# Performance work log

Hardware: AMD Instinct MI355X
Metric: run time of the kernel (lower is better)

The kernel has to match this reference:

```python
import jax, jax.numpy as jnp
import numpy as np

EMBED_DIM = 768
N_HEADS = 12
HEAD_DIM = EMBED_DIM // N_HEADS
B, S = 8, 1024


def setup_inputs() -> dict:
    key = jax.random.key(0)
    ks = jax.random.split(key, 7)
    sc = 1.0 / np.sqrt(HEAD_DIM)
    return {
        "sequences": jax.random.normal(ks[0], (B, S, EMBED_DIM), dtype=jnp.float32),
        # per-head Linear weights stored [H, in, out] (torch Linear is x @ W.T + b;
        # with random init the layout convention is equivalent math)
        "Wq": jax.random.normal(ks[1], (N_HEADS, HEAD_DIM, HEAD_DIM), dtype=jnp.float32) * sc,
        "bq": jax.random.normal(ks[2], (N_HEADS, HEAD_DIM), dtype=jnp.float32) * 0.01,
        "Wk": jax.random.normal(ks[3], (N_HEADS, HEAD_DIM, HEAD_DIM), dtype=jnp.float32) * sc,
        "bk": jax.random.normal(ks[4], (N_HEADS, HEAD_DIM), dtype=jnp.float32) * 0.01,
        "Wv": jax.random.normal(ks[5], (N_HEADS, HEAD_DIM, HEAD_DIM), dtype=jnp.float32) * sc,
        "bv": jax.random.normal(ks[6], (N_HEADS, HEAD_DIM), dtype=jnp.float32) * 0.01,
    }


def reference(sequences, Wq, bq, Wk, bk, Wv, bv):
    b, s, d = sequences.shape
    h, hd = Wq.shape[0], Wq.shape[1]
    x = sequences.reshape(b, s, h, hd)              # split embed dim into heads
    q = jnp.einsum("bshd,hde->bshe", x, Wq) + bq    # per-head linear (block-diag GEMM)
    k = jnp.einsum("bshd,hde->bshe", x, Wk) + bk
    v = jnp.einsum("bshd,hde->bshe", x, Wv) + bv
    # NOTE: original module applies NO 1/sqrt(head_dim) scaling
    logits = jnp.einsum("bshe,bthe->bhst", q, k)    # [B,H,S,S]
    attn = jax.nn.softmax(logits, axis=-1)
    out = jnp.einsum("bhst,bthe->bshe", attn, v)    # [B,S,H,hd]
    return out.reshape(b, s, d)
```

## Files before the change

kernel.cpp:

```cpp
#include <hip/hip_runtime.h>
#include <stdint.h>

#define EMBED 768
#define NH 12
#define HD 64
#define Bsz 8
#define Ssz 1024
#define LOG2E 1.44269504088896f

typedef __attribute__((ext_vector_type(4))) float f32x4;
typedef __attribute__((ext_vector_type(8))) _Float16 f16x8;
typedef __attribute__((ext_vector_type(4))) _Float16 f16x4;
typedef __attribute__((ext_vector_type(2))) _Float16 f16x2;

__device__ __forceinline__ int SW(int row, int col) {
    return row * 64 + (col ^ ((row & 7) << 3));
}

__launch_bounds__(256)
__global__ void qkv_proj(const float* __restrict__ x,
                         const float* __restrict__ Wq, const float* __restrict__ bq,
                         const float* __restrict__ Wk, const float* __restrict__ bk,
                         const float* __restrict__ Wv, const float* __restrict__ bv,
                         _Float16* __restrict__ Qb, _Float16* __restrict__ Kb,
                         _Float16* __restrict__ Vt)
{
    __shared__ _Float16 XT[128 * 72];
    __shared__ _Float16 Wt[3 * 64 * 72];
    __shared__ float Bs[192];

    const int bt = blockIdx.x;
    const int st = bt & 7;
    const int h  = (bt >> 3) % NH;
    const int b  = bt / (8 * NH);
    const int sbase = st * 128;
    const int tid = threadIdx.x;
    const int lane = tid & 63, w = tid >> 6;
    const int l15 = lane & 15, quad = lane >> 4;

    for (int i = 0; i < 8; ++i) {
        int idx = tid + 256 * i;
        int row = idx >> 4;
        int c4  = (idx & 15) * 4;
        const float4 g = *(const float4*)&x[(size_t)(b * Ssz + sbase + row) * EMBED + h * HD + c4];
        f16x4 v; v[0] = (_Float16)g.x; v[1] = (_Float16)g.y; v[2] = (_Float16)g.z; v[3] = (_Float16)g.w;
        *(f16x4*)&XT[row * 72 + c4] = v;
    }
    {
        const float* Ws0[3] = {Wq, Wk, Wv};
        const float* bs0[3] = {bq, bk, bv};
#pragma unroll
        for (int m = 0; m < 3; ++m) {
            const float* W = Ws0[m] + (size_t)h * HD * HD;
            for (int i = 0; i < 4; ++i) {
                int idx = tid + 256 * i;
                int d = idx >> 4, e4 = (idx & 15) * 4;
                float4 g = *(const float4*)&W[d * 64 + e4];
                Wt[m * 4608 + (e4 + 0) * 72 + d] = (_Float16)g.x;
                Wt[m * 4608 + (e4 + 1) * 72 + d] = (_Float16)g.y;
                Wt[m * 4608 + (e4 + 2) * 72 + d] = (_Float16)g.z;
                Wt[m * 4608 + (e4 + 3) * 72 + d] = (_Float16)g.w;
            }
        }
        if (tid < 192) Bs[tid] = bs0[tid >> 6][h * HD + (tid & 63)];
    }
    __syncthreads();

    f16x8 bx[2][2];
    const int nbg0 = w * 2;
#pragma unroll
    for (int nb = 0; nb < 2; ++nb)
#pragma unroll
        for (int kh = 0; kh < 2; ++kh)
            bx[nb][kh] = *(const f16x8*)&XT[((nbg0 + nb) * 16 + l15) * 72 + kh * 32 + quad * 8];
    __syncthreads();

    const size_t qkbase = (size_t)(b * NH + h) * Ssz + sbase;
    const f32x4 zero = {0.f, 0.f, 0.f, 0.f};

#pragma unroll
    for (int m = 0; m < 3; ++m) {
        f32x4 acc[2][4];
#pragma unroll
        for (int nb = 0; nb < 2; ++nb)
#pragma unroll
            for (int eb = 0; eb < 4; ++eb) acc[nb][eb] = zero;
#pragma unroll
        for (int eb = 0; eb < 4; ++eb)
#pragma unroll
            for (int kh = 0; kh < 2; ++kh) {
                f16x8 aw = *(const f16x8*)&Wt[m * 4608 + (eb * 16 + l15) * 72 + kh * 32 + quad * 8];
#pragma unroll
                for (int nb = 0; nb < 2; ++nb)
                    acc[nb][eb] = __builtin_amdgcn_mfma_f32_16x16x32_f16(aw, bx[nb][kh], acc[nb][eb], 0, 0, 0);
            }

        if (m < 2) {
            const float sc = (m == 0) ? LOG2E : 1.0f;
#pragma unroll
            for (int nb = 0; nb < 2; ++nb)
#pragma unroll
                for (int eb = 0; eb < 4; ++eb) {
                    f32x4 bb = *(const f32x4*)&Bs[m * 64 + eb * 16 + quad * 4];
                    f16x4 v;
#pragma unroll
                    for (int r = 0; r < 4; ++r) v[r] = (_Float16)((acc[nb][eb][r] + bb[r]) * sc);
                    *(f16x4*)&XT[((nbg0 + nb) * 16 + l15) * 72 + eb * 16 + quad * 4] = v;
                }
            __syncthreads();
            _Float16* outp = (m == 0) ? Qb : Kb;
            for (int i = 0; i < 4; ++i) {
                int idx = tid + 256 * i;
                int s = idx >> 3, e8 = (idx & 7) * 8;
                *(f16x8*)&outp[(qkbase + s) * HD + e8] = *(const f16x8*)&XT[s * 72 + e8];
            }
            __syncthreads();
        } else {
            _Float16* Vs = XT;
#pragma unroll
            for (int nb = 0; nb < 2; ++nb)
#pragma unroll
                for (int eb = 0; eb < 4; ++eb) {
                    f32x4 bb = *(const f32x4*)&Bs[128 + eb * 16 + quad * 4];
#pragma unroll
                    for (int r = 0; r < 4; ++r)
                        Vs[(eb * 16 + quad * 4 + r) * 136 + (nbg0 + nb) * 16 + l15] =
                            (_Float16)(acc[nb][eb][r] + bb[r]);
                }
            __syncthreads();
            for (int i = 0; i < 4; ++i) {
                int idx = tid + 256 * i;
                int e = idx >> 4, s8 = (idx & 15) * 8;
                *(f16x8*)&Vt[((size_t)(b * NH + h) * 64 + e) * Ssz + sbase + s8] =
                    *(const f16x8*)&Vs[e * 136 + s8];
            }
        }
    }
}

__launch_bounds__(512)
__global__ void attn(const _Float16* __restrict__ Qb, const _Float16* __restrict__ Kb,
                     const _Float16* __restrict__ Vt, float* __restrict__ out)
{
    __shared__ _Float16 KV[2 * 8192];
    __shared__ _Float16 Pl[8 * 16 * 64];

    const int bt = blockIdx.x;
    const int hh = bt % 96;
    const int qt = bt / 96;
    const int h  = hh % NH;
    const int b  = hh / NH;

    const int tid = threadIdx.x;
    const int lane = tid & 63, w = tid >> 6;
    const int l15 = lane & 15, quad = lane >> 4;

    const size_t bh = (size_t)(b * NH + h);
    const _Float16* Qg = Qb + bh * Ssz * HD;
    const _Float16* Kg = Kb + bh * Ssz * HD;
    const _Float16* Vg = Vt + bh * (size_t)HD * Ssz;

    const int qrow0 = qt * 128 + w * 16;
    f16x8 aq[2];
#pragma unroll
    for (int kh = 0; kh < 2; ++kh)
        aq[kh] = *(const f16x8*)&Qg[(qrow0 + l15) * HD + kh * 32 + quad * 8];

    const f32x4 zero = {0.f, 0.f, 0.f, 0.f};
    f32x4 o[4];
#pragma unroll
    for (int eb = 0; eb < 4; ++eb) o[eb] = zero;
    float m_run = -INFINITY, l_run = 0.f;

    const int srow = tid >> 3;
    const int scol = (tid & 7) * 8;
    const int swst = SW(srow, scol);

    f16x8 kr = *(const f16x8*)&Kg[srow * HD + scol];
    f16x8 vr = *(const f16x8*)&Vg[(size_t)srow * Ssz + scol];
    *(f16x8*)&KV[swst] = kr;
    *(f16x8*)&KV[4096 + swst] = vr;
    __syncthreads();

    _Float16* Pw = &Pl[w * 1024];
    const int swq = (l15 & 7) << 3;

    for (int kt = 0; kt < 16; ++kt) {
        const int cur = kt & 1;
        if (kt < 15) {
            kr = *(const f16x8*)&Kg[((kt + 1) * 64 + srow) * HD + scol];
            vr = *(const f16x8*)&Vg[(size_t)srow * Ssz + (kt + 1) * 64 + scol];
        }
        const _Float16* Ksb = &KV[cur * 8192];
        const _Float16* Vsb = &KV[cur * 8192 + 4096];

        f32x4 st[4];
#pragma unroll
        for (int tb = 0; tb < 4; ++tb) {
            f32x4 acc = zero;
#pragma unroll
            for (int kh = 0; kh < 2; ++kh) {
                f16x8 ak = *(const f16x8*)&Ksb[SW(tb * 16 + l15, kh * 32 + quad * 8)];
                acc = __builtin_amdgcn_mfma_f32_16x16x32_f16(ak, aq[kh], acc, 0, 0, 0);
            }
            st[tb] = acc;
        }

        float mt = st[0][0];
#pragma unroll
        for (int tb = 0; tb < 4; ++tb)
#pragma unroll
            for (int r = 0; r < 4; ++r) mt = fmaxf(mt, st[tb][r]);
        mt = fmaxf(mt, __shfl_xor(mt, 16, 64));
        mt = fmaxf(mt, __shfl_xor(mt, 32, 64));
        float mn = fmaxf(m_run, mt);
        float al = __builtin_amdgcn_exp2f(m_run - mn);
        float rs = 0.f;
        f16x4 pv[4];
#pragma unroll
        for (int tb = 0; tb < 4; ++tb) {
            float p0 = __builtin_amdgcn_exp2f(st[tb][0] - mn);
            float p1 = __builtin_amdgcn_exp2f(st[tb][1] - mn);
            float p2 = __builtin_amdgcn_exp2f(st[tb][2] - mn);
            float p3 = __builtin_amdgcn_exp2f(st[tb][3] - mn);
            rs += (p0 + p1) + (p2 + p3);
            f16x2 lo = __builtin_bit_cast(f16x2, __builtin_amdgcn_cvt_pkrtz(p0, p1));
            f16x2 hi = __builtin_bit_cast(f16x2, __builtin_amdgcn_cvt_pkrtz(p2, p3));
            pv[tb][0] = lo[0]; pv[tb][1] = lo[1]; pv[tb][2] = hi[0]; pv[tb][3] = hi[1];
        }
        rs += __shfl_xor(rs, 16, 64);
        rs += __shfl_xor(rs, 32, 64);
        l_run = l_run * al + rs;
        m_run = mn;
#pragma unroll
        for (int eb = 0; eb < 4; ++eb) o[eb] *= al;

#pragma unroll
        for (int tb = 0; tb < 4; ++tb)
            *(f16x4*)&Pw[l15 * 64 + ((tb * 16 + quad * 4) ^ swq)] = pv[tb];
        __asm__ __volatile__("s_waitcnt lgkmcnt(0)" ::: "memory");
        f16x8 bp[2];
#pragma unroll
        for (int kh = 0; kh < 2; ++kh)
            bp[kh] = *(const f16x8*)&Pw[l15 * 64 + ((kh * 32 + quad * 8) ^ swq)];

#pragma unroll
        for (int kh = 0; kh < 2; ++kh)
#pragma unroll
            for (int eb = 0; eb < 4; ++eb) {
                f16x8 av = *(const f16x8*)&Vsb[SW(eb * 16 + l15, kh * 32 + quad * 8)];
                o[eb] = __builtin_amdgcn_mfma_f32_16x16x32_f16(av, bp[kh], o[eb], 0, 0, 0);
            }

        if (kt < 15) {
            const int nxt = cur ^ 1;
            *(f16x8*)&KV[nxt * 8192 + swst] = kr;
            *(f16x8*)&KV[nxt * 8192 + 4096 + swst] = vr;
        }
        __syncthreads();
    }

    const float inv = 1.f / l_run;
    const int q = qrow0 + l15;
    float* op = &out[(size_t)(b * Ssz + q) * EMBED + h * HD + quad * 4];
#pragma unroll
    for (int eb = 0; eb < 4; ++eb) {
        f32x4 r = o[eb] * inv;
        *(f32x4*)&op[eb * 16] = r;
    }
}

extern "C" void kernel_launch(void* const* d_in, const int* in_sizes, int n_in,
                              void* d_out, int out_size, void* d_ws, size_t ws_size,
                              hipStream_t stream) {
    const float* x  = (const float*)d_in[0];
    const float* Wq = (const float*)d_in[1];
    const float* bq = (const float*)d_in[2];
    const float* Wk = (const float*)d_in[3];
    const float* bk = (const float*)d_in[4];
    const float* Wv = (const float*)d_in[5];
    const float* bv = (const float*)d_in[6];

    _Float16* Qb = (_Float16*)d_ws;
    _Float16* Kb = Qb + (size_t)Bsz * NH * Ssz * HD;
    _Float16* Vt = Kb + (size_t)Bsz * NH * Ssz * HD;

    qkv_proj<<<dim3(Bsz * NH * 8), dim3(256), 0, stream>>>(x, Wq, bq, Wk, bk, Wv, bv, Qb, Kb, Vt);
    attn<<<dim3(Bsz * NH * 8), dim3(512), 0, stream>>>(Qb, Kb, Vt, (float*)d_out);
}
```

Before: 136.7 us.

## Compute softmax row sums via extra MFMA ones-row and move KV stores earlier

Replaces the explicit per-row softmax sum (adds plus cross-lane shuffles) with a fifth MFMA against a ones row appended to the V tile in shared memory, so the denominator accumulates in o[4]. It also moves the next-tile K/V shared-memory stores before the P-read wait, so they can overlap with the PV MFMAs. The cost is an extra MFMA per k-half per tile, larger LDS buffers, and the sum is now taken over fp16-rounded probabilities rather than fp32 ones.

```diff
diff --git a/kernel.cpp b/kernel.cpp
--- a/kernel.cpp
+++ b/kernel.cpp
@@ -138,11 +138,12 @@
     }
 }
 
+#define KVBUF 9216
 __launch_bounds__(512)
 __global__ void attn(const _Float16* __restrict__ Qb, const _Float16* __restrict__ Kb,
                      const _Float16* __restrict__ Vt, float* __restrict__ out)
 {
-    __shared__ _Float16 KV[2 * 8192];
+    __shared__ _Float16 KV[2 * KVBUF];
     __shared__ _Float16 Pl[8 * 16 * 64];
 
     const int bt = blockIdx.x;
@@ -167,14 +168,24 @@
         aq[kh] = *(const f16x8*)&Qg[(qrow0 + l15) * HD + kh * 32 + quad * 8];
 
     const f32x4 zero = {0.f, 0.f, 0.f, 0.f};
-    f32x4 o[4];
-#pragma unroll
-    for (int eb = 0; eb < 4; ++eb) o[eb] = zero;
-    float m_run = -INFINITY, l_run = 0.f;
+    f32x4 o[5];
+#pragma unroll
+    for (int eb = 0; eb < 5; ++eb) o[eb] = zero;
+    float m_run = -INFINITY;
 
     const int srow = tid >> 3;
     const int scol = (tid & 7) * 8;
     const int swst = SW(srow, scol);
+
+    {
+        int bufi = tid >> 8;
+        int r16  = (tid >> 4) & 15;
+        int c4   = (tid & 15) * 4;
+        f16x4 v;
+        _Float16 val = (r16 == 0) ? (_Float16)1.0f : (_Float16)0.0f;
+        v[0] = val; v[1] = val; v[2] = val; v[3] = val;
+        *(f16x4*)&KV[bufi * KVBUF + 4096 + SW(64 + r16, c4)] = v;
+    }
 
     f16x8 kr = *(const f16x8*)&Kg[srow * HD + scol];
     f16x8 vr = *(const f16x8*)&Vg[(size_t)srow * Ssz + scol];
@@ -191,8 +202,8 @@
             kr = *(const f16x8*)&Kg[((kt + 1) * 64 + srow) * HD + scol];
             vr = *(const f16x8*)&Vg[(size_t)srow * Ssz + (kt + 1) * 64 + scol];
         }
-        const _Float16* Ksb = &KV[cur * 8192];
-        const _Float16* Vsb = &KV[cur * 8192 + 4096];
+        const _Float16* Ksb = &KV[cur * KVBUF];
+        const _Float16* Vsb = &KV[cur * KVBUF + 4096];
 
         f32x4 st[4];
 #pragma unroll
@@ -215,7 +226,7 @@
         mt = fmaxf(mt, __shfl_xor(mt, 32, 64));
         float mn = fmaxf(m_run, mt);
         float al = __builtin_amdgcn_exp2f(m_run - mn);
-        float rs = 0.f;
+        m_run = mn;
         f16x4 pv[4];
 #pragma unroll
         for (int tb = 0; tb < 4; ++tb) {
@@ -223,21 +234,20 @@
             float p1 = __builtin_amdgcn_exp2f(st[tb][1] - mn);
             float p2 = __builtin_amdgcn_exp2f(st[tb][2] - mn);
             float p3 = __builtin_amdgcn_exp2f(st[tb][3] - mn);
-            rs += (p0 + p1) + (p2 + p3);
             f16x2 lo = __builtin_bit_cast(f16x2, __builtin_amdgcn_cvt_pkrtz(p0, p1));
             f16x2 hi = __builtin_bit_cast(f16x2, __builtin_amdgcn_cvt_pkrtz(p2, p3));
             pv[tb][0] = lo[0]; pv[tb][1] = lo[1]; pv[tb][2] = hi[0]; pv[tb][3] = hi[1];
         }
-        rs += __shfl_xor(rs, 16, 64);
-        rs += __shfl_xor(rs, 32, 64);
-        l_run = l_run * al + rs;
-        m_run = mn;
-#pragma unroll
-        for (int eb = 0; eb < 4; ++eb) o[eb] *= al;
 
 #pragma unroll
         for (int tb = 0; tb < 4; ++tb)
             *(f16x4*)&Pw[l15 * 64 + ((tb * 16 + quad * 4) ^ swq)] = pv[tb];
+
+        if (kt < 15) {
+            const int nxt = cur ^ 1;
+            *(f16x8*)&KV[nxt * KVBUF + swst] = kr;
+            *(f16x8*)&KV[nxt * KVBUF + 4096 + swst] = vr;
+        }
         __asm__ __volatile__("s_waitcnt lgkmcnt(0)" ::: "memory");
         f16x8 bp[2];
 #pragma unroll
@@ -245,22 +255,21 @@
             bp[kh] = *(const f16x8*)&Pw[l15 * 64 + ((kh * 32 + quad * 8) ^ swq)];
 
 #pragma unroll
+        for (int eb = 0; eb < 5; ++eb) o[eb] *= al;
+
+#pragma unroll
         for (int kh = 0; kh < 2; ++kh)
 #pragma unroll
-            for (int eb = 0; eb < 4; ++eb) {
+            for (int eb = 0; eb < 5; ++eb) {
                 f16x8 av = *(const f16x8*)&Vsb[SW(eb * 16 + l15, kh * 32 + quad * 8)];
                 o[eb] = __builtin_amdgcn_mfma_f32_16x16x32_f16(av, bp[kh], o[eb], 0, 0, 0);
             }
 
-        if (kt < 15) {
-            const int nxt = cur ^ 1;
-            *(f16x8*)&KV[nxt * 8192 + swst] = kr;
-            *(f16x8*)&KV[nxt * 8192 + 4096 + swst] = vr;
-        }
         __syncthreads();
     }
 
-    const float inv = 1.f / l_run;
+    const float lv = __shfl(o[4][0], l15, 64);
+    const float inv = 1.f / lv;
     const int q = qrow0 + l15;
     float* op = &out[(size_t)(b * Ssz + q) * EMBED + h * HD + quad * 4];
 #pragma unroll
```

New measurement: 133.5 us. 2.3% less time.
